# Kernel optimization log

Hardware: AMD Instinct MI355X
Metric: run time of the kernel (lower is better)

Reference implementation:

```python
import jax, jax.numpy as jnp
import numpy as np

AUX_LOSS_COEFF = 0.03125  # config.aux_loss_coeff


def setup_inputs() -> dict:
    key = jax.random.key(0)
    k0, k1 = jax.random.split(key, 2)
    B, T, d, m = 2, 2048, 2048, 16384
    activations = jax.random.normal(k0, (B, T, d), dtype=jnp.float32)
    # kaiming-uniform-ish init, then unit-norm rows (as in _initialize_weights)
    W_enc = jax.random.normal(k1, (m, d), dtype=jnp.float32)
    W_enc = W_enc / (jnp.linalg.norm(W_enc, axis=1, keepdims=True) + 1e-8)
    b_enc = jnp.zeros((m,), dtype=jnp.float32)
    W_emb = W_enc.T  # tied init: W_emb.weight = W_enc.weight.T, shape [d, m]
    steps_since_active = jnp.zeros((m,), dtype=jnp.int32)  # buffer, starts at 0
    return {
        "activations": activations,
        "W_enc": W_enc,
        "b_enc": b_enc,
        "W_emb": W_emb,
        "steps_since_active": steps_since_active,
        "topk": 64,
        "dead_window": 1000,
    }


def reference(activations, W_enc, b_enc, W_emb, steps_since_active, topk, dead_window):
    B, T, d = activations.shape
    m = W_enc.shape[0]
    # pre_act = W_enc(activations)  -> [B, T, m]
    pre_act = jnp.einsum("btd,md->btm", activations, W_enc) + b_enc
    # top-k over concept dim
    top_vals, top_idx = jax.lax.top_k(pre_act, topk)  # [B, T, k]
    # sparse = zeros scatter top_vals at top_idx along last dim
    flat_idx = top_idx.reshape(-1, topk)   # [B*T, k]
    flat_vals = top_vals.reshape(-1, topk)
    rows = jnp.arange(flat_idx.shape[0])[:, None]
    sparse = (
        jnp.zeros((flat_idx.shape[0], m), dtype=pre_act.dtype)
        .at[rows, flat_idx]
        .set(flat_vals)
        .reshape(B, T, m)
    )
    # encoded = W_emb(sparse) -> [B, T, d]
    encoded = jnp.einsum("btm,dm->btd", sparse, W_emb)
    # aux loss on dead concepts (dead_mask all False at init -> 0.0)
    dead_mask = (steps_since_active >= dead_window).astype(pre_act.dtype)  # [m]
    n_dead = jnp.sum(dead_mask)
    denom = jnp.maximum(n_dead * B * T, 1.0)
    dead_mean = jnp.sum(pre_act * dead_mask) / denom
    aux_loss = jnp.where(n_dead > 0, -dead_mean * AUX_LOSS_COEFF, jnp.zeros((), pre_act.dtype))
    return encoded, aux_loss
```

## Files before the change

kernel.cpp:

```cpp
#include <hip/hip_runtime.h>
#include <cfloat>
#include <climits>


typedef __attribute__((ext_vector_type(8))) short short8;
typedef __attribute__((ext_vector_type(4))) float f32x4;

#define NC      96
#define KFIN    64
#define TAU     1e-3f
#define AUXC    0.03125f
#define MCONC   16384
#define DDIM    2048
#define CAP     768

__device__ __forceinline__ ushort f2bf(float f) {
  unsigned u = __float_as_uint(f);
  u += 0x7fff + ((u >> 16) & 1);
  return (ushort)(u >> 16);
}
__device__ __forceinline__ float bf2f(ushort h) {
  return __uint_as_float(((unsigned)h) << 16);
}

__global__ void k_init(float* dead_sum, int* n_dead, int* wl_count) {
  *dead_sum = 0.f;
  *n_dead = 0;
  *wl_count = 0;
}

__global__ void k_count_dead(const int* __restrict__ steps, const int* __restrict__ dw,
                             int m, int* __restrict__ n_dead) {
  int i = blockIdx.x * blockDim.x + threadIdx.x;
  if (i < m && steps[i] >= *dw) atomicAdd(n_dead, 1);
}

__global__ void k_final(const float* __restrict__ ds, const int* __restrict__ nd,
                        float* __restrict__ outp, float BT) {
  int n = *nd;
  float denom = fmaxf((float)n * BT, 1.0f);
  outp[0] = (n > 0) ? -((*ds) / denom) * AUXC : 0.0f;
}

__global__ __launch_bounds__(256)
void k_prep(const float* __restrict__ srcA, ushort* __restrict__ dstA, int totA,
            const float* __restrict__ srcB, ushort* __restrict__ dstB, int totB,
            int K,
            const float* __restrict__ Wemb, ushort* __restrict__ WembT,
            int d, int m, int nstage) {
  __shared__ float tile[32][33];
  const int b = blockIdx.x;
  if (b < nstage) {
    int idx = b * 256 + threadIdx.x;
    const float* src;
    ushort* dst;
    int t;
    if (idx < totA) { src = srcA; dst = dstA; t = idx; }
    else if (idx < totA + totB) { src = srcB; dst = dstB; t = idx - totA; }
    else return;
    int nch = K >> 5;
    int row = t / nch, c = t - row * nch;
    const float* s = src + (size_t)row * K + c * 32;
    float f[32];
#pragma unroll
    for (int q = 0; q < 8; ++q) *(float4*)&f[q * 4] = *(const float4*)(s + q * 4);
    ushort hi[32];
    float lof[32];
#pragma unroll
    for (int e = 0; e < 32; ++e) {
      hi[e] = f2bf(f[e]);
      lof[e] = f[e] - bf2f(hi[e]);
    }
    ushort* dd = dst + (size_t)row * ((size_t)K * 2) + c * 64;
#pragma unroll
    for (int q = 0; q < 4; ++q) {
      short8 o;
#pragma unroll
      for (int e = 0; e < 8; ++e) o[e] = (short)hi[q * 8 + e];
      *(short8*)(dd + q * 8) = o;
    }
#pragma unroll
    for (int q = 0; q < 4; ++q) {
      short8 o;
#pragma unroll
      for (int e = 0; e < 8; ++e) o[e] = (short)f2bf(lof[q * 8 + e]);
      *(short8*)(dd + 32 + q * 8) = o;
    }
    return;
  }
  const int tb = b - nstage;
  const int nmb = m >> 5;
  const int mb = (tb % nmb) * 32, db = (tb / nmb) * 32;
  const int tx = threadIdx.x & 31, ty = threadIdx.x >> 5;
#pragma unroll
  for (int i = 0; i < 32; i += 8)
    tile[ty + i][tx] = Wemb[(size_t)(db + ty + i) * m + mb + tx];
  __syncthreads();
#pragma unroll
  for (int i = 0; i < 32; i += 8)
    WembT[(size_t)(mb + ty + i) * d + db + tx] = f2bf(tile[tx][ty + i]);
}

__device__ __forceinline__ void gload16(const void* g, void* l) {
  __builtin_amdgcn_global_load_lds((const __attribute__((address_space(1))) void*)g,
                                   (__attribute__((address_space(3))) void*)l, 16, 0, 0);
}

__global__ __launch_bounds__(512, 2)
void k_gemm3(const ushort* __restrict__ Ast, const ushort* __restrict__ Bst,
             const float* __restrict__ bias, float* __restrict__ C,
             int row0, int K, int m, int nbm) {
  __shared__ ushort As[2][256 * 64];
  __shared__ ushort Bs[2][256 * 64];
  const int tid = threadIdx.x;
  const int lane = tid & 63, w = tid >> 6;
  const int wm = w >> 2, wn = w & 3;

  const int nbn = m >> 8;
  const int nwg = nbm * nbn;
  const int q = nwg >> 3, r = nwg & 7;
  const int x = blockIdx.x & 7, i0 = blockIdx.x >> 3;
  const int wg = (x < r) ? x * (q + 1) + i0 : r * (q + 1) + (x - r) * q + i0;
  const int bm = wg / nbn, bn = wg % nbn;

  const size_t K2 = (size_t)K * 2;
  const int nch = K >> 5;

  const int gr = lane >> 3;
  const int swz = (((lane & 7) ^ gr) << 3);
  const size_t arow0 = (size_t)(row0 + bm * 256);
  const size_t brow0 = (size_t)(bn * 256);

  f32x4 acc[8][4];
#pragma unroll
  for (int i = 0; i < 8; ++i)
#pragma unroll
    for (int j = 0; j < 4; ++j) acc[i][j] = (f32x4)(0.f);

  const int kg = lane >> 4;
  const int j7 = lane & 7;
  const int sh = ((kg ^ j7) << 3);
  const int rbase = (lane & 15) * 64;

  auto STAGE_A = [&](int buf, int c) {
#pragma unroll
    for (int t = 0; t < 4; ++t) {
      int i = w * 4 + t;
      int rr = i * 8 + gr;
      gload16(Ast + (arow0 + rr) * K2 + (size_t)c * 64 + swz, (void*)(As[buf] + i * 512));
    }
  };
  auto STAGE_B = [&](int buf, int c) {
#pragma unroll
    for (int t = 0; t < 4; ++t) {
      int i = w * 4 + t;
      int rr = i * 8 + gr;
      gload16(Bst + (brow0 + rr) * K2 + (size_t)c * 64 + swz, (void*)(Bs[buf] + i * 512));
    }
  };

  STAGE_A(0, 0);
  STAGE_B(0, 0);
  __syncthreads();

  int cur = 0;
  for (int j = 0; j < nch; ++j) {
    short8 bh[4], bl[4];
#pragma unroll
    for (int ph = 0; ph < 4; ++ph) {
      if (ph == 0) {
#pragma unroll
        for (int fn = 0; fn < 4; ++fn) {
          const ushort* pb = Bs[cur] + (wn * 64 + fn * 16) * 64 + rbase;
          bh[fn] = *(const short8*)(pb + sh);
          bl[fn] = *(const short8*)(pb + (sh ^ 32));
        }
      }
      const ushort* pa0 = As[cur] + (wm * 128 + (2 * ph + 0) * 16) * 64 + rbase;
      const ushort* pa1 = As[cur] + (wm * 128 + (2 * ph + 1) * 16) * 64 + rbase;
      short8 ah0 = *(const short8*)(pa0 + sh);
      short8 al0 = *(const short8*)(pa0 + (sh ^ 32));
      short8 ah1 = *(const short8*)(pa1 + sh);
      short8 al1 = *(const short8*)(pa1 + (sh ^ 32));
      if (j + 1 < nch) {
        if (ph == 0) STAGE_A(cur ^ 1, j + 1);
        else if (ph == 1) STAGE_B(cur ^ 1, j + 1);
      }
      __builtin_amdgcn_s_barrier();
      __builtin_amdgcn_s_setprio(1);
#pragma unroll
      for (int fn = 0; fn < 4; ++fn) {
        acc[2 * ph + 0][fn] = __builtin_amdgcn_mfma_f32_16x16x32_bf16(ah0, bh[fn], acc[2 * ph + 0][fn], 0, 0, 0);
        acc[2 * ph + 0][fn] = __builtin_amdgcn_mfma_f32_16x16x32_bf16(ah0, bl[fn], acc[2 * ph + 0][fn], 0, 0, 0);
        acc[2 * ph + 0][fn] = __builtin_amdgcn_mfma_f32_16x16x32_bf16(al0, bh[fn], acc[2 * ph + 0][fn], 0, 0, 0);
        acc[2 * ph + 1][fn] = __builtin_amdgcn_mfma_f32_16x16x32_bf16(ah1, bh[fn], acc[2 * ph + 1][fn], 0, 0, 0);
        acc[2 * ph + 1][fn] = __builtin_amdgcn_mfma_f32_16x16x32_bf16(ah1, bl[fn], acc[2 * ph + 1][fn], 0, 0, 0);
        acc[2 * ph + 1][fn] = __builtin_amdgcn_mfma_f32_16x16x32_bf16(al1, bh[fn], acc[2 * ph + 1][fn], 0, 0, 0);
      }
      __builtin_amdgcn_s_setprio(0);
      __builtin_amdgcn_s_barrier();
    }
    __syncthreads();
    cur ^= 1;
  }

  const int orow = bm * 256 + wm * 128;
  const int ocol = bn * 256 + wn * 64;
#pragma unroll
  for (int fn = 0; fn < 4; ++fn) {
    float bb = bias[ocol + fn * 16 + (lane & 15)];
#pragma unroll
    for (int fm = 0; fm < 8; ++fm) {
      int rb = orow + fm * 16 + (lane >> 4) * 4;
#pragma unroll
      for (int rr = 0; rr < 4; ++rr)
        __builtin_nontemporal_store(acc[fm][fn][rr] + bb,
            &C[(size_t)(rb + rr) * m + ocol + fn * 16 + (lane & 15)]);
    }
  }
}

__global__ __launch_bounds__(256)
void k_topk(const float* __restrict__ preact, int row0,
            const int* __restrict__ steps, const int* __restrict__ dw,
            const int* __restrict__ topk_d,
            float* __restrict__ cvals, int* __restrict__ cidx,
            float* __restrict__ dead_sum,
            int* __restrict__ rowflag, int* __restrict__ wl, int* __restrict__ wl_count,
            float* __restrict__ tvals, int* __restrict__ tidx) {
  __shared__ float dred[4];
  __shared__ float wmx[4], wmn[4];
  __shared__ float sm1[4], sm2[4];
  __shared__ int scnt;
  __shared__ int pos;
  __shared__ float cval_s[CAP];
  __shared__ int cidx_s[CAP];
  __shared__ float vk1_s, vk_s;
  __shared__ int flag_s;
  const int tid = threadIdx.x;
  const int lane = tid & 63;
  const int grow = row0 + blockIdx.x;
  const float* pr = preact + (size_t)blockIdx.x * MCONC;

  int kt = *topk_d;
  if (kt > KFIN) kt = KFIN;
  if (kt < 1) kt = 1;

  float v[64];
#pragma unroll
  for (int c = 0; c < 16; ++c) {
    const f32x4* p4 = (const f32x4*)(pr + (size_t)c * 1024 + tid * 4);
    f32x4 t4 = __builtin_nontemporal_load(p4);
    v[c * 4 + 0] = t4[0]; v[c * 4 + 1] = t4[1];
    v[c * 4 + 2] = t4[2]; v[c * 4 + 3] = t4[3];
  }

  int dwv = *dw;
  float ds = 0.f;
#pragma unroll
  for (int c = 0; c < 16; ++c) {
    int4 st = *(const int4*)(steps + c * 1024 + tid * 4);
    if (st.x >= dwv) ds += v[c * 4 + 0];
    if (st.y >= dwv) ds += v[c * 4 + 1];
    if (st.z >= dwv) ds += v[c * 4 + 2];
    if (st.w >= dwv) ds += v[c * 4 + 3];
  }
  for (int off = 32; off; off >>= 1) ds += __shfl_down(ds, off);
  if (lane == 0) dred[tid >> 6] = ds;

  float mx = -FLT_MAX, mn = FLT_MAX, s1 = 0.f, s2 = 0.f;
#pragma unroll
  for (int i = 0; i < 64; ++i) {
    mx = fmaxf(mx, v[i]); mn = fminf(mn, v[i]);
    s1 += v[i]; s2 = fmaf(v[i], v[i], s2);
  }
  for (int off = 32; off; off >>= 1) {
    mx = fmaxf(mx, __shfl_xor(mx, off));
    mn = fminf(mn, __shfl_xor(mn, off));
    s1 += __shfl_xor(s1, off);
    s2 += __shfl_xor(s2, off);
  }
  if (lane == 0) { wmx[tid >> 6] = mx; wmn[tid >> 6] = mn; sm1[tid >> 6] = s1; sm2[tid >> 6] = s2; }
  __syncthreads();
  if (tid == 0) {
    float t = dred[0] + dred[1] + dred[2] + dred[3];
    if (t != 0.f) atomicAdd(dead_sum, t);
  }
  float row_mx = fmaxf(fmaxf(wmx[0], wmx[1]), fmaxf(wmx[2], wmx[3]));
  float row_mn = fminf(fminf(wmn[0], wmn[1]), fminf(wmn[2], wmn[3]));
  float T1 = sm1[0] + sm1[1] + sm1[2] + sm1[3];
  float T2 = sm2[0] + sm2[1] + sm2[2] + sm2[3];
  float mu = T1 * (1.f / 16384.f);
  float var = fmaxf(T2 * (1.f / 16384.f) - mu * mu, 0.f);
  float mid = mu + 2.0f * sqrtf(var);

  float lo = row_mn - 1.0f, hi = row_mx;
  float t = lo;
  bool found = false;
  for (int it = 0; it < 23 && !found; ++it) {
    __syncthreads();
    if (tid == 0) scnt = 0;
    __syncthreads();
    int cl = 0;
#pragma unroll
    for (int i = 0; i < 64; ++i) cl += (v[i] > mid);
    for (int off = 32; off; off >>= 1) cl += __shfl_xor(cl, off);
    if (lane == 0) atomicAdd(&scnt, cl);
    __syncthreads();
    int cnt = scnt;
    if (cnt >= NC && cnt <= CAP) { t = mid; found = true; }
    else if (cnt < NC) hi = mid;
    else lo = mid;
    mid = 0.5f * (lo + hi);
  }
  if (!found) t = lo;

  __syncthreads();
  if (tid == 0) pos = 0;
  __syncthreads();
#pragma unroll
  for (int i = 0; i < 64; ++i) {
    if (v[i] > t) {
      int p = atomicAdd(&pos, 1);
      if (p < CAP) {
        cval_s[p] = v[i];
        cidx_s[p] = ((i >> 2) << 10) | (tid << 2) | (i & 3);
      }
    }
  }
  __syncthreads();
  int Cn = pos < CAP ? pos : CAP;

  int rnk[3];
  float mvv[3];
  int mii[3];
#pragma unroll
  for (int jj = 0; jj < 3; ++jj) {
    int j = tid + jj * 256;
    rnk[jj] = INT_MAX;
    if (j < Cn) {
      float my = cval_s[j];
      int myidx = cidx_s[j];
      int rank = 0;
      for (int c = 0; c < Cn; ++c) {
        float o = cval_s[c];
        rank += (o > my) || (o == my && cidx_s[c] < myidx);
      }
      rnk[jj] = rank; mvv[jj] = my; mii[jj] = myidx;
      if (rank < NC) {
        cvals[(size_t)grow * NC + rank] = my;
        cidx[(size_t)grow * NC + rank] = myidx;
      }
      if (rank == kt - 1) vk1_s = my;
      if (rank == kt)     vk_s  = my;
    }
  }
  __syncthreads();
  if (tid == 0) {
    int f = (vk1_s - vk_s < TAU) ? 1 : 0;
    rowflag[grow] = f;
    flag_s = f;
    if (f) { int p = atomicAdd(wl_count, 1); wl[p] = grow; }
  }
  __syncthreads();
  if (!flag_s) {
#pragma unroll
    for (int jj = 0; jj < 3; ++jj) {
      if (rnk[jj] < kt) {
        tvals[(size_t)grow * KFIN + rnk[jj]] = mvv[jj];
        tidx[(size_t)grow * KFIN + rnk[jj]] = mii[jj];
      }
    }
  }
}

__global__ __launch_bounds__(256)
void k_dots(const int* __restrict__ wl, const int* __restrict__ wl_count,
            const int* __restrict__ cidx, const float* __restrict__ act,
            const float* __restrict__ Wenc, const float* __restrict__ bias,
            double* __restrict__ dv, int d) {
  __shared__ float arow[DDIM];
  const int total = (*wl_count) * 8;
  const int lane = threadIdx.x & 63, w = threadIdx.x >> 6;
  for (int b = blockIdx.x; b < total; b += gridDim.x) {
    const int row = wl[b >> 3], part = b & 7;
    __syncthreads();
    for (int i = threadIdx.x; i < d; i += 256) arow[i] = act[(size_t)row * d + i];
    __syncthreads();
#pragma unroll
    for (int cc = 0; cc < 3; ++cc) {
      int c = part * 12 + w * 3 + cc;
      int ci = cidx[(size_t)row * NC + c];
      const float* wrow = Wenc + (size_t)ci * d;
      double s = 0.0;
      for (int i = lane; i < d; i += 64)
        s += (double)arow[i] * (double)wrow[i];
      for (int off = 32; off; off >>= 1) s += __shfl_down(s, off);
      if (lane == 0) dv[(size_t)row * NC + c] = s + (double)bias[ci];
    }
  }
}

__global__ __launch_bounds__(128)
void k_select(const float* __restrict__ cvals, const int* __restrict__ cidx,
              const int* __restrict__ rowflag, const double* __restrict__ dv,
              const int* __restrict__ topk_d,
              float* __restrict__ tvals, int* __restrict__ tidx) {
  const int row = blockIdx.x, tid = threadIdx.x;
  if (!rowflag[row]) return;
  int kt = *topk_d;
  if (kt > KFIN) kt = KFIN;
  if (kt < 1) kt = 1;
  __shared__ double sdv[NC];
  if (tid < NC) sdv[tid] = dv[(size_t)row * NC + tid];
  __syncthreads();
  if (tid < NC) {
    double my = sdv[tid];
    int rank = 0;
#pragma unroll 8
    for (int c = 0; c < NC; ++c) {
      double v = sdv[c];
      rank += (v > my) || (v == my && c < tid);
    }
    if (rank < kt) {
      tvals[(size_t)row * KFIN + rank] = cvals[(size_t)row * NC + tid];
      tidx[(size_t)row * KFIN + rank] = cidx[(size_t)row * NC + tid];
    }
  }
}

__global__ __launch_bounds__(256)
void k_decode_t(const float* __restrict__ tvals, const int* __restrict__ tidx,
                const int* __restrict__ topk_d, const ushort* __restrict__ Wt,
                float* __restrict__ out, int d) {
  __shared__ float sv[KFIN];
  __shared__ int si[KFIN];
  const int row = blockIdx.x, tid = threadIdx.x;
  int kt = *topk_d;
  if (kt > KFIN) kt = KFIN;
  if (tid < kt) {
    sv[tid] = tvals[(size_t)row * KFIN + tid];
    si[tid] = tidx[(size_t)row * KFIN + tid];
  }
  __syncthreads();
  for (int base = tid * 8; base < d; base += 2048) {
    float a0 = 0, a1 = 0, a2 = 0, a3 = 0, a4 = 0, a5 = 0, a6 = 0, a7 = 0;
#pragma unroll 4
    for (int j = 0; j < kt; ++j) {
      float vv = sv[j];
      short8 wv = *(const short8*)(Wt + (size_t)si[j] * d + base);
      a0 = fmaf(vv, bf2f((ushort)wv[0]), a0);
      a1 = fmaf(vv, bf2f((ushort)wv[1]), a1);
      a2 = fmaf(vv, bf2f((ushort)wv[2]), a2);
      a3 = fmaf(vv, bf2f((ushort)wv[3]), a3);
      a4 = fmaf(vv, bf2f((ushort)wv[4]), a4);
      a5 = fmaf(vv, bf2f((ushort)wv[5]), a5);
      a6 = fmaf(vv, bf2f((ushort)wv[6]), a6);
      a7 = fmaf(vv, bf2f((ushort)wv[7]), a7);
    }
    float* o = out + (size_t)row * d + base;
    *(float4*)o = make_float4(a0, a1, a2, a3);
    *(float4*)(o + 4) = make_float4(a4, a5, a6, a7);
  }
}

__global__ __launch_bounds__(256)
void k_decode_g(const float* __restrict__ tvals, const int* __restrict__ tidx,
                const int* __restrict__ topk_d, const float* __restrict__ Wemb,
                float* __restrict__ out, int d, int m) {
  __shared__ float sv[KFIN];
  __shared__ int si[KFIN];
  const int row = blockIdx.x, tid = threadIdx.x;
  int kt = *topk_d;
  if (kt > KFIN) kt = KFIN;
  if (tid < kt) {
    sv[tid] = tvals[(size_t)row * KFIN + tid];
    si[tid] = tidx[(size_t)row * KFIN + tid];
  }
  __syncthreads();
  for (int base = tid * 8; base < d; base += 2048) {
    float acc[8] = {0, 0, 0, 0, 0, 0, 0, 0};
    for (int j = 0; j < kt; ++j) {
      float vv = sv[j];
      int ix = si[j];
#pragma unroll
      for (int e = 0; e < 8; ++e)
        acc[e] = fmaf(vv, Wemb[(size_t)(base + e) * m + ix], acc[e]);
    }
    float* o = out + (size_t)row * d + base;
    *(float4*)o = *(float4*)&acc[0];
    *(float4*)(o + 4) = *(float4*)&acc[4];
  }
}

extern "C" void kernel_launch(void* const* d_in, const int* in_sizes, int n_in,
                              void* d_out, int out_size, void* d_ws, size_t ws_size,
                              hipStream_t stream) {
  const float* act   = (const float*)d_in[0];
  const float* Wenc  = (const float*)d_in[1];
  const float* benc  = (const float*)d_in[2];
  const float* Wemb  = (const float*)d_in[3];
  const int*   steps = (const int*)d_in[4];
  const int*   topk  = (const int*)d_in[5];
  const int*   dwin  = (const int*)d_in[6];
  const int m = in_sizes[2];
  const int d = in_sizes[1] / m;
  const int rows = in_sizes[0] / d;
  float* out = (float*)d_out;

  char* ws = (char*)d_ws;
  float* dead_sum = (float*)ws;
  int*   n_dead   = (int*)(ws + 8);
  int*   wl_count = (int*)(ws + 16);
  size_t off = 256;
  float* cvals = (float*)(ws + off); off += (size_t)rows * NC * 4;
  int*   cidx  = (int*)(ws + off);   off += (size_t)rows * NC * 4;
  float* tvals = (float*)(ws + off); off += (size_t)rows * KFIN * 4;
  int*   tidx  = (int*)(ws + off);   off += (size_t)rows * KFIN * 4;
  int*   rowflag = (int*)(ws + off); off += (size_t)rows * 4;
  int*   wl      = (int*)(ws + off); off += (size_t)rows * 4;
  double* dv     = (double*)(ws + off); off += (size_t)rows * NC * 8;
  ushort* Ast  = (ushort*)(ws + off); off += (size_t)rows * d * 4;
  ushort* Bst  = (ushort*)(ws + off); off += (size_t)m * d * 4;

  const size_t wembT_bytes = (size_t)m * d * sizeof(ushort);
  const size_t row_bytes = (size_t)m * sizeof(float);
  size_t avail = (ws_size > off) ? ws_size - off : 0;

  ushort* WembT = nullptr;
  if (avail >= wembT_bytes + 256 * row_bytes) {
    WembT = (ushort*)(ws + off);
    off += wembT_bytes;
    avail -= wembT_bytes;
  }
  int chunk = (int)(avail / row_bytes);
  if (chunk > rows) chunk = rows;
  chunk &= ~255;
  if (chunk < 256) chunk = 256;
  float* preact = (float*)(ws + off);

  k_init<<<1, 1, 0, stream>>>(dead_sum, n_dead, wl_count);
  k_count_dead<<<(m + 255) / 256, 256, 0, stream>>>(steps, dwin, m, n_dead);

  int totA = rows * (d >> 5);
  int totB = m * (d >> 5);
  int nstage = (totA + totB + 255) / 256;
  int ntrans = WembT ? (m / 32) * (d / 32) : 0;
  k_prep<<<nstage + ntrans, 256, 0, stream>>>(act, Ast, totA, Wenc, Bst, totB, d,
                                              Wemb, WembT, d, m, nstage);

  for (int r0 = 0; r0 < rows; r0 += chunk) {
    int cr = rows - r0;
    if (cr > chunk) cr = chunk;
    int nbm = cr / 256;
    int nwg = nbm * (m / 256);
    k_gemm3<<<nwg, 512, 0, stream>>>(Ast, Bst, benc, preact, r0, d, m, nbm);
    k_topk<<<cr, 256, 0, stream>>>(preact, r0, steps, dwin, topk,
                                   cvals, cidx, dead_sum,
                                   rowflag, wl, wl_count, tvals, tidx);
  }

  k_dots<<<rows, 256, 0, stream>>>(wl, wl_count, cidx, act, Wenc, benc, dv, d);
  k_select<<<rows, 128, 0, stream>>>(cvals, cidx, rowflag, dv, topk, tvals, tidx);

  if (WembT) {
    k_decode_t<<<rows, 256, 0, stream>>>(tvals, tidx, topk, WembT, out, d);
  } else {
    k_decode_g<<<rows, 256, 0, stream>>>(tvals, tidx, topk, Wemb, out, d, m);
  }

  k_final<<<1, 1, 0, stream>>>(dead_sum, n_dead, out + (size_t)rows * d, (float)rows);
}
```

Baseline: 1.151 ms.

## Switch split-precision GEMM from bf16x3 to fp16 with a single-precision weight operand

The encoder GEMM previously split both operands into bf16 hi/lo parts and ran three MFMAs per tile. It now splits only the activations into fp16 hi/lo, keeps W_enc as one fp16 copy, and runs two fp16 MFMAs per tile. This halves B-operand staging bytes, LDS footprint and prep work, and cuts matrix-core work by a third. In exchange, accuracy on W_enc drops to fp16, so the top-k candidate refinement tolerance TAU is doubled to cover the larger error. That looser margin may send more rows to the exact fallback path.

```diff
diff --git a/kernel.cpp b/kernel.cpp
--- a/kernel.cpp
+++ b/kernel.cpp
@@ -8,7 +8,7 @@
 
 #define NC      96
 #define KFIN    64
-#define TAU     1e-3f
+#define TAU     2e-3f
 #define AUXC    0.03125f
 #define MCONC   16384
 #define DDIM    2048
@@ -21,6 +21,16 @@
 }
 __device__ __forceinline__ float bf2f(ushort h) {
   return __uint_as_float(((unsigned)h) << 16);
+}
+__device__ __forceinline__ ushort f2h(float f) {
+  union { _Float16 h; ushort u; } cv;
+  cv.h = (_Float16)f;
+  return cv.u;
+}
+__device__ __forceinline__ float h2f(ushort u) {
+  union { _Float16 h; ushort u; } cv;
+  cv.u = u;
+  return (float)cv.h;
 }
 
 __global__ void k_init(float* dead_sum, int* n_dead, int* wl_count) {
@@ -52,39 +62,53 @@
   const int b = blockIdx.x;
   if (b < nstage) {
     int idx = b * 256 + threadIdx.x;
-    const float* src;
-    ushort* dst;
-    int t;
-    if (idx < totA) { src = srcA; dst = dstA; t = idx; }
-    else if (idx < totA + totB) { src = srcB; dst = dstB; t = idx - totA; }
-    else return;
     int nch = K >> 5;
-    int row = t / nch, c = t - row * nch;
-    const float* s = src + (size_t)row * K + c * 32;
-    float f[32];
-#pragma unroll
-    for (int q = 0; q < 8; ++q) *(float4*)&f[q * 4] = *(const float4*)(s + q * 4);
-    ushort hi[32];
-    float lof[32];
-#pragma unroll
-    for (int e = 0; e < 32; ++e) {
-      hi[e] = f2bf(f[e]);
-      lof[e] = f[e] - bf2f(hi[e]);
-    }
-    ushort* dd = dst + (size_t)row * ((size_t)K * 2) + c * 64;
-#pragma unroll
-    for (int q = 0; q < 4; ++q) {
-      short8 o;
-#pragma unroll
-      for (int e = 0; e < 8; ++e) o[e] = (short)hi[q * 8 + e];
-      *(short8*)(dd + q * 8) = o;
-    }
-#pragma unroll
-    for (int q = 0; q < 4; ++q) {
-      short8 o;
-#pragma unroll
-      for (int e = 0; e < 8; ++e) o[e] = (short)f2bf(lof[q * 8 + e]);
-      *(short8*)(dd + 32 + q * 8) = o;
+    if (idx < totA) {
+      int t = idx;
+      int row = t / nch, c = t - row * nch;
+      const float* s = srcA + (size_t)row * K + c * 32;
+      float f[32];
+#pragma unroll
+      for (int qq = 0; qq < 8; ++qq) *(float4*)&f[qq * 4] = *(const float4*)(s + qq * 4);
+      ushort hi[32];
+#pragma unroll
+      for (int e = 0; e < 32; ++e) hi[e] = f2h(f[e]);
+      ushort* dd = dstA + (size_t)row * ((size_t)K * 2) + c * 64;
+#pragma unroll
+      for (int qq = 0; qq < 4; ++qq) {
+        short8 o;
+#pragma unroll
+        for (int e = 0; e < 8; ++e) o[e] = (short)hi[qq * 8 + e];
+        *(short8*)(dd + qq * 8) = o;
+      }
+#pragma unroll
+      for (int qq = 0; qq < 4; ++qq) {
+        short8 o;
+#pragma unroll
+        for (int e = 0; e < 8; ++e) {
+          int ix = qq * 8 + e;
+          o[e] = (short)f2h(f[ix] - h2f(hi[ix]));
+        }
+        *(short8*)(dd + 32 + qq * 8) = o;
+      }
+      return;
+    }
+    if (idx < totA + totB) {
+      int t = idx - totA;
+      int row = t / nch, c = t - row * nch;
+      const float* s = srcB + (size_t)row * K + c * 32;
+      float f[32];
+#pragma unroll
+      for (int qq = 0; qq < 8; ++qq) *(float4*)&f[qq * 4] = *(const float4*)(s + qq * 4);
+      ushort* dd = dstB + (size_t)row * (size_t)K + c * 32;
+#pragma unroll
+      for (int qq = 0; qq < 4; ++qq) {
+        short8 o;
+#pragma unroll
+        for (int e = 0; e < 8; ++e) o[e] = (short)f2h(f[qq * 8 + e]);
+        *(short8*)(dd + qq * 8) = o;
+      }
+      return;
     }
     return;
   }
@@ -111,7 +135,7 @@
              const float* __restrict__ bias, float* __restrict__ C,
              int row0, int K, int m, int nbm) {
   __shared__ ushort As[2][256 * 64];
-  __shared__ ushort Bs[2][256 * 64];
+  __shared__ ushort Bs[2][256 * 32];
   const int tid = threadIdx.x;
   const int lane = tid & 63, w = tid >> 6;
   const int wm = w >> 2, wn = w & 3;
@@ -124,10 +148,14 @@
   const int bm = wg / nbn, bn = wg % nbn;
 
   const size_t K2 = (size_t)K * 2;
+  const size_t KB = (size_t)K;
   const int nch = K >> 5;
 
-  const int gr = lane >> 3;
-  const int swz = (((lane & 7) ^ gr) << 3);
+  const int grA = lane >> 3;
+  const int swzA = (((lane & 7) ^ grA) << 3);
+  const int grB = lane >> 2;
+  const int swzB = (((lane & 3) ^ ((lane >> 4) & 3)) << 3);
+
   const size_t arow0 = (size_t)(row0 + bm * 256);
   const size_t brow0 = (size_t)(bn * 256);
 
@@ -138,24 +166,25 @@
     for (int j = 0; j < 4; ++j) acc[i][j] = (f32x4)(0.f);
 
   const int kg = lane >> 4;
-  const int j7 = lane & 7;
-  const int sh = ((kg ^ j7) << 3);
-  const int rbase = (lane & 15) * 64;
+  const int shA = ((kg ^ (lane & 7)) << 3);
+  const int rbaseA = (lane & 15) * 64;
+  const int shB = ((kg ^ ((lane >> 2) & 3)) << 3);
+  const int rbaseB = (lane & 15) * 32;
 
   auto STAGE_A = [&](int buf, int c) {
 #pragma unroll
     for (int t = 0; t < 4; ++t) {
       int i = w * 4 + t;
-      int rr = i * 8 + gr;
-      gload16(Ast + (arow0 + rr) * K2 + (size_t)c * 64 + swz, (void*)(As[buf] + i * 512));
+      int rr = i * 8 + grA;
+      gload16(Ast + (arow0 + rr) * K2 + (size_t)c * 64 + swzA, (void*)(As[buf] + i * 512));
     }
   };
   auto STAGE_B = [&](int buf, int c) {
 #pragma unroll
-    for (int t = 0; t < 4; ++t) {
-      int i = w * 4 + t;
-      int rr = i * 8 + gr;
-      gload16(Bst + (brow0 + rr) * K2 + (size_t)c * 64 + swz, (void*)(Bs[buf] + i * 512));
+    for (int t = 0; t < 2; ++t) {
+      int i = w * 2 + t;
+      int rr = i * 16 + grB;
+      gload16(Bst + (brow0 + rr) * KB + (size_t)c * 32 + swzB, (void*)(Bs[buf] + i * 512));
     }
   };
 
@@ -165,23 +194,22 @@
 
   int cur = 0;
   for (int j = 0; j < nch; ++j) {
-    short8 bh[4], bl[4];
+    short8 bh[4];
 #pragma unroll
     for (int ph = 0; ph < 4; ++ph) {
       if (ph == 0) {
 #pragma unroll
         for (int fn = 0; fn < 4; ++fn) {
-          const ushort* pb = Bs[cur] + (wn * 64 + fn * 16) * 64 + rbase;
-          bh[fn] = *(const short8*)(pb + sh);
-          bl[fn] = *(const short8*)(pb + (sh ^ 32));
+          const ushort* pb = Bs[cur] + (wn * 64 + fn * 16) * 32 + rbaseB;
+          bh[fn] = *(const short8*)(pb + shB);
         }
       }
-      const ushort* pa0 = As[cur] + (wm * 128 + (2 * ph + 0) * 16) * 64 + rbase;
-      const ushort* pa1 = As[cur] + (wm * 128 + (2 * ph + 1) * 16) * 64 + rbase;
-      short8 ah0 = *(const short8*)(pa0 + sh);
-      short8 al0 = *(const short8*)(pa0 + (sh ^ 32));
-      short8 ah1 = *(const short8*)(pa1 + sh);
-      short8 al1 = *(const short8*)(pa1 + (sh ^ 32));
+      const ushort* pa0 = As[cur] + (wm * 128 + (2 * ph + 0) * 16) * 64 + rbaseA;
+      const ushort* pa1 = As[cur] + (wm * 128 + (2 * ph + 1) * 16) * 64 + rbaseA;
+      short8 ah0 = *(const short8*)(pa0 + shA);
+      short8 al0 = *(const short8*)(pa0 + (shA ^ 32));
+      short8 ah1 = *(const short8*)(pa1 + shA);
+      short8 al1 = *(const short8*)(pa1 + (shA ^ 32));
       if (j + 1 < nch) {
         if (ph == 0) STAGE_A(cur ^ 1, j + 1);
         else if (ph == 1) STAGE_B(cur ^ 1, j + 1);
@@ -190,12 +218,10 @@
       __builtin_amdgcn_s_setprio(1);
 #pragma unroll
       for (int fn = 0; fn < 4; ++fn) {
-        acc[2 * ph + 0][fn] = __builtin_amdgcn_mfma_f32_16x16x32_bf16(ah0, bh[fn], acc[2 * ph + 0][fn], 0, 0, 0);
-        acc[2 * ph + 0][fn] = __builtin_amdgcn_mfma_f32_16x16x32_bf16(ah0, bl[fn], acc[2 * ph + 0][fn], 0, 0, 0);
-        acc[2 * ph + 0][fn] = __builtin_amdgcn_mfma_f32_16x16x32_bf16(al0, bh[fn], acc[2 * ph + 0][fn], 0, 0, 0);
-        acc[2 * ph + 1][fn] = __builtin_amdgcn_mfma_f32_16x16x32_bf16(ah1, bh[fn], acc[2 * ph + 1][fn], 0, 0, 0);
-        acc[2 * ph + 1][fn] = __builtin_amdgcn_mfma_f32_16x16x32_bf16(ah1, bl[fn], acc[2 * ph + 1][fn], 0, 0, 0);
-        acc[2 * ph + 1][fn] = __builtin_amdgcn_mfma_f32_16x16x32_bf16(al1, bh[fn], acc[2 * ph + 1][fn], 0, 0, 0);
+        acc[2 * ph + 0][fn] = __builtin_amdgcn_mfma_f32_16x16x32_f16(ah0, bh[fn], acc[2 * ph + 0][fn], 0, 0, 0);
+        acc[2 * ph + 0][fn] = __builtin_amdgcn_mfma_f32_16x16x32_f16(al0, bh[fn], acc[2 * ph + 0][fn], 0, 0, 0);
+        acc[2 * ph + 1][fn] = __builtin_amdgcn_mfma_f32_16x16x32_f16(ah1, bh[fn], acc[2 * ph + 1][fn], 0, 0, 0);
+        acc[2 * ph + 1][fn] = __builtin_amdgcn_mfma_f32_16x16x32_f16(al1, bh[fn], acc[2 * ph + 1][fn], 0, 0, 0);
       }
       __builtin_amdgcn_s_setprio(0);
       __builtin_amdgcn_s_barrier();
@@ -521,7 +547,7 @@
   int*   wl      = (int*)(ws + off); off += (size_t)rows * 4;
   double* dv     = (double*)(ws + off); off += (size_t)rows * NC * 8;
   ushort* Ast  = (ushort*)(ws + off); off += (size_t)rows * d * 4;
-  ushort* Bst  = (ushort*)(ws + off); off += (size_t)m * d * 4;
+  ushort* Bst  = (ushort*)(ws + off); off += (size_t)m * d * 2;
 
   const size_t wembT_bytes = (size_t)m * d * sizeof(ushort);
   const size_t row_bytes = (size_t)m * sizeof(float);
```

Result: faster. 1.099 ms (-4.5%).
